# Performance work log

Hardware: AMD Instinct MI355X
Metric: run time of the kernel (lower is better)

The kernel has to match this reference:

```python
import jax, jax.numpy as jnp
import numpy as np
import math

ALPHA_MIN = math.exp(-1.0 / 5.0)   # ~0.8187
ALPHA_MAX = math.exp(-1.0 / 25.0)  # ~0.9608
THRESHOLD = 1.0


def setup_inputs() -> dict:
    key = jax.random.key(0)
    k1, k2, k3, k4, k5 = jax.random.split(key, 5)
    B, T, I, H = 32, 2048, 256, 512
    x = jax.random.normal(k1, (B, T, I), dtype=jnp.float32)
    # Linear weight, kaiming-ish scale
    W = jax.random.normal(k2, (H, I), dtype=jnp.float32) * (1.0 / np.sqrt(I))
    # alpha ~ U[exp(-1/5), exp(-1/25)] as in nn.init.uniform_
    alpha = ALPHA_MIN + jax.random.uniform(k3, (H,), dtype=jnp.float32) * (ALPHA_MAX - ALPHA_MIN)
    # initial membrane potential / spike state (torch.rand in _lif_cell)
    u0 = jax.random.uniform(k4, (B, H), dtype=jnp.float32)
    s0 = jax.random.uniform(k5, (B, H), dtype=jnp.float32)
    return {"x": x, "W": W, "alpha": alpha, "u0": u0, "s0": s0}


def reference(x, W, alpha, u0, s0):
    # clamp alpha to its admissible range (lif_feature has no 'NoClamp')
    alpha = jnp.clip(alpha, ALPHA_MIN, ALPHA_MAX)
    b = 1.0 - alpha  # lif_feature has no 'B'

    # feedforward projection: [B, T, H]
    Wx = jnp.einsum('bti,hi->bth', x, W)

    def step(carry, wx_t):
        ut, st = carry
        ut = alpha * (ut - st) + b * wx_t          # leaky integrate + soft reset
        st = (ut - THRESHOLD > 0).astype(ut.dtype)  # heaviside spike
        return (ut, st), st

    # scan over time: Wx -> [T, B, H]
    _, s = jax.lax.scan(step, (u0, s0), jnp.swapaxes(Wx, 0, 1))
    return jnp.swapaxes(s, 0, 1)  # [B, T, H]
```

## Files before the change

### kernel.cpp

```cpp
#include <hip/hip_runtime.h>
#include <hip/hip_bf16.h>

#define ALPHA_MIN 0.8187307530779818f
#define ALPHA_MAX 0.9607894391523232f

typedef _Float16 f16;
typedef _Float16 f16x8 __attribute__((ext_vector_type(8)));
typedef float f32x16 __attribute__((ext_vector_type(16)));

#define LDSTRIDE 40

__global__ __launch_bounds__(256, 2) void gemm_f16x3(
    const float* __restrict__ X,
    const float* __restrict__ W,
    float* __restrict__ C,
    int M, int N, int K)
{
    __shared__ f16 Ah[128 * LDSTRIDE];
    __shared__ f16 Al[128 * LDSTRIDE];
    __shared__ f16 Bh[128 * LDSTRIDE];
    __shared__ f16 Bl[128 * LDSTRIDE];

    const int tid = threadIdx.x;
    const int mt = blockIdx.x >> 2;
    const int nt = blockIdx.x & 3;
    const int m0 = mt * 128, n0 = nt * 128;

    const int lane = tid & 63;
    const int wv   = tid >> 6;
    const int wm   = wv & 1;
    const int wn   = wv >> 1;
    const int fm   = lane & 31;
    const int fq   = lane >> 5;

    const int srow = tid >> 2;
    const int sc8  = tid & 3;

    f32x16 accH[2][2], accL[2][2];
#pragma unroll
    for (int i = 0; i < 2; ++i)
#pragma unroll
        for (int j = 0; j < 2; ++j)
#pragma unroll
            for (int e = 0; e < 16; ++e) { accH[i][j][e] = 0.0f; accL[i][j][e] = 0.0f; }

    const int KT = K / 32;
    for (int kt = 0; kt < KT; ++kt) {
#pragma unroll
        for (int i = 0; i < 2; ++i) {
            const int row = srow + 64 * i;
            {
                const float* src = X + (size_t)(m0 + row) * K + kt * 32 + sc8 * 8;
                float4 v0 = *(const float4*)(src);
                float4 v1 = *(const float4*)(src + 4);
                float vin[8] = {v0.x, v0.y, v0.z, v0.w, v1.x, v1.y, v1.z, v1.w};
                f16x8 hv, lv;
#pragma unroll
                for (int j = 0; j < 8; ++j) {
                    f16 hj = (f16)vin[j];
                    hv[j] = hj;
                    lv[j] = (f16)((vin[j] - (float)hj) * 2048.0f);
                }
                *(f16x8*)&Ah[row * LDSTRIDE + sc8 * 8] = hv;
                *(f16x8*)&Al[row * LDSTRIDE + sc8 * 8] = lv;
            }
            {
                const float* src = W + (size_t)(n0 + row) * K + kt * 32 + sc8 * 8;
                float4 v0 = *(const float4*)(src);
                float4 v1 = *(const float4*)(src + 4);
                float vin[8] = {v0.x, v0.y, v0.z, v0.w, v1.x, v1.y, v1.z, v1.w};
                f16x8 hv, lv;
#pragma unroll
                for (int j = 0; j < 8; ++j) {
                    f16 hj = (f16)vin[j];
                    hv[j] = hj;
                    lv[j] = (f16)((vin[j] - (float)hj) * 2048.0f);
                }
                *(f16x8*)&Bh[row * LDSTRIDE + sc8 * 8] = hv;
                *(f16x8*)&Bl[row * LDSTRIDE + sc8 * 8] = lv;
            }
        }
        __syncthreads();

#pragma unroll
        for (int ks = 0; ks < 2; ++ks) {
            f16x8 af[2][2], bf[2][2];
#pragma unroll
            for (int mb = 0; mb < 2; ++mb) {
                const int ro = (wm * 64 + mb * 32 + fm) * LDSTRIDE + ks * 16 + fq * 8;
                af[mb][0] = *(const f16x8*)&Ah[ro];
                af[mb][1] = *(const f16x8*)&Al[ro];
            }
#pragma unroll
            for (int nb = 0; nb < 2; ++nb) {
                const int ro = (wn * 64 + nb * 32 + fm) * LDSTRIDE + ks * 16 + fq * 8;
                bf[nb][0] = *(const f16x8*)&Bh[ro];
                bf[nb][1] = *(const f16x8*)&Bl[ro];
            }
#pragma unroll
            for (int mb = 0; mb < 2; ++mb)
#pragma unroll
                for (int nb = 0; nb < 2; ++nb) {
                    accH[mb][nb] = __builtin_amdgcn_mfma_f32_32x32x16_f16(af[mb][0], bf[nb][0], accH[mb][nb], 0, 0, 0);
                    accL[mb][nb] = __builtin_amdgcn_mfma_f32_32x32x16_f16(af[mb][0], bf[nb][1], accL[mb][nb], 0, 0, 0);
                    accL[mb][nb] = __builtin_amdgcn_mfma_f32_32x32x16_f16(af[mb][1], bf[nb][0], accL[mb][nb], 0, 0, 0);
                }
        }
        __syncthreads();
    }

#pragma unroll
    for (int mb = 0; mb < 2; ++mb)
#pragma unroll
        for (int nb = 0; nb < 2; ++nb) {
            const int col   = n0 + wn * 64 + nb * 32 + fm;
            const int rbase = m0 + wm * 64 + mb * 32 + 4 * fq;
#pragma unroll
            for (int g = 0; g < 4; ++g)
#pragma unroll
                for (int r = 0; r < 4; ++r) {
                    const int row = rbase + 8 * g + r;
                    const float v = accH[mb][nb][4 * g + r]
                                  + accL[mb][nb][4 * g + r] * (1.0f / 2048.0f);
                    C[(size_t)row * N + col] = v;
                }
        }
}

#define SU 64

__global__ __launch_bounds__(64) void lif_scan(
    float* __restrict__ buf,
    const float* __restrict__ alpha,
    const float* __restrict__ u0,
    const float* __restrict__ s0,
    int T, int H)
{
    const int chain = blockIdx.x * 64 + threadIdx.x;
    const int h = chain % H;
    const int b = chain / H;

    float a = alpha[h];
    a = fminf(fmaxf(a, ALPHA_MIN), ALPHA_MAX);
    const float bb = 1.0f - a;

    float u = u0[chain];
    float s = s0[chain];

    float* base = buf + (size_t)b * T * H + h;

    float w0[SU], w1[SU];
#pragma unroll
    for (int j = 0; j < SU; ++j) w0[j] = base[(size_t)j * H];

    const int NC = T / SU;
    for (int c = 0; c < NC; c += 2) {
#pragma unroll
        for (int j = 0; j < SU; ++j) w1[j] = base[(size_t)((c + 1) * SU + j) * H];
#pragma unroll
        for (int j = 0; j < SU; ++j) {
            const float d = u - s;
            u = fmaf(a, d, bb * w0[j]);
            s = (u > 1.0f) ? 1.0f : 0.0f;
            base[(size_t)(c * SU + j) * H] = s;
        }
        if (c + 2 < NC) {
#pragma unroll
            for (int j = 0; j < SU; ++j) w0[j] = base[(size_t)((c + 2) * SU + j) * H];
        }
#pragma unroll
        for (int j = 0; j < SU; ++j) {
            const float d = u - s;
            u = fmaf(a, d, bb * w1[j]);
            s = (u > 1.0f) ? 1.0f : 0.0f;
            base[(size_t)((c + 1) * SU + j) * H] = s;
        }
    }
}

extern "C" void kernel_launch(void* const* d_in, const int* in_sizes, int n_in,
                              void* d_out, int out_size, void* d_ws, size_t ws_size,
                              hipStream_t stream) {
    const float* x     = (const float*)d_in[0];
    const float* W     = (const float*)d_in[1];
    const float* alpha = (const float*)d_in[2];
    const float* u0    = (const float*)d_in[3];
    const float* s0    = (const float*)d_in[4];
    float* out = (float*)d_out;

    const int H = in_sizes[2];
    const int I = in_sizes[1] / H;
    const int B = in_sizes[3] / H;
    const int T = in_sizes[0] / (B * I);
    const int M = B * T;

    const int grid = (M / 128) * (H / 128);
    gemm_f16x3<<<grid, 256, 0, stream>>>(x, W, out, M, H, I);

    lif_scan<<<(B * H) / 64, 64, 0, stream>>>(out, alpha, u0, s0, T, H);
}
```

Baseline: 302.9 us.

## Pre-split inputs into fp16 hi/lo buffers before GEMM, scan out-of-place

```diff
diff --git a/kernel.cpp b/kernel.cpp
--- a/kernel.cpp
+++ b/kernel.cpp
@@ -8,13 +8,32 @@
 typedef _Float16 f16x8 __attribute__((ext_vector_type(8)));
 typedef float f32x16 __attribute__((ext_vector_type(16)));
 
+__global__ __launch_bounds__(256) void convert_split(
+    const float* __restrict__ src,
+    f16* __restrict__ hi, f16* __restrict__ lo, int n8)
+{
+    const int i = blockIdx.x * 256 + threadIdx.x;
+    if (i >= n8) return;
+    const float4 v0 = ((const float4*)src)[2 * i];
+    const float4 v1 = ((const float4*)src)[2 * i + 1];
+    const float v[8] = {v0.x, v0.y, v0.z, v0.w, v1.x, v1.y, v1.z, v1.w};
+    f16x8 h, l;
+#pragma unroll
+    for (int j = 0; j < 8; ++j) {
+        const f16 hj = (f16)v[j];
+        h[j] = hj;
+        l[j] = (f16)((v[j] - (float)hj) * 2048.0f);
+    }
+    ((f16x8*)hi)[i] = h;
+    ((f16x8*)lo)[i] = l;
+}
+
 #define LDSTRIDE 40
 
-__global__ __launch_bounds__(256, 2) void gemm_f16x3(
-    const float* __restrict__ X,
-    const float* __restrict__ W,
-    float* __restrict__ C,
-    int M, int N, int K)
+__global__ __launch_bounds__(256, 2) void gemm_f16pre(
+    const f16* __restrict__ Xh, const f16* __restrict__ Xl,
+    const f16* __restrict__ Wh, const f16* __restrict__ Wl,
+    float* __restrict__ C, int M, int N, int K)
 {
     __shared__ f16 Ah[128 * LDSTRIDE];
     __shared__ f16 Al[128 * LDSTRIDE];
@@ -49,36 +68,13 @@
 #pragma unroll
         for (int i = 0; i < 2; ++i) {
             const int row = srow + 64 * i;
-            {
-                const float* src = X + (size_t)(m0 + row) * K + kt * 32 + sc8 * 8;
-                float4 v0 = *(const float4*)(src);
-                float4 v1 = *(const float4*)(src + 4);
-                float vin[8] = {v0.x, v0.y, v0.z, v0.w, v1.x, v1.y, v1.z, v1.w};
-                f16x8 hv, lv;
-#pragma unroll
-                for (int j = 0; j < 8; ++j) {
-                    f16 hj = (f16)vin[j];
-                    hv[j] = hj;
-                    lv[j] = (f16)((vin[j] - (float)hj) * 2048.0f);
-                }
-                *(f16x8*)&Ah[row * LDSTRIDE + sc8 * 8] = hv;
-                *(f16x8*)&Al[row * LDSTRIDE + sc8 * 8] = lv;
-            }
-            {
-                const float* src = W + (size_t)(n0 + row) * K + kt * 32 + sc8 * 8;
-                float4 v0 = *(const float4*)(src);
-                float4 v1 = *(const float4*)(src + 4);
-                float vin[8] = {v0.x, v0.y, v0.z, v0.w, v1.x, v1.y, v1.z, v1.w};
-                f16x8 hv, lv;
-#pragma unroll
-                for (int j = 0; j < 8; ++j) {
-                    f16 hj = (f16)vin[j];
-                    hv[j] = hj;
-                    lv[j] = (f16)((vin[j] - (float)hj) * 2048.0f);
-                }
-                *(f16x8*)&Bh[row * LDSTRIDE + sc8 * 8] = hv;
-                *(f16x8*)&Bl[row * LDSTRIDE + sc8 * 8] = lv;
-            }
+            const size_t gx = (size_t)(m0 + row) * K + kt * 32 + sc8 * 8;
+            const size_t gw = (size_t)(n0 + row) * K + kt * 32 + sc8 * 8;
+            const int lo_ = row * LDSTRIDE + sc8 * 8;
+            *(f16x8*)&Ah[lo_] = *(const f16x8*)&Xh[gx];
+            *(f16x8*)&Al[lo_] = *(const f16x8*)&Xl[gx];
+            *(f16x8*)&Bh[lo_] = *(const f16x8*)&Wh[gw];
+            *(f16x8*)&Bl[lo_] = *(const f16x8*)&Wl[gw];
         }
         __syncthreads();
 
@@ -120,17 +116,17 @@
 #pragma unroll
                 for (int r = 0; r < 4; ++r) {
                     const int row = rbase + 8 * g + r;
-                    const float v = accH[mb][nb][4 * g + r]
-                                  + accL[mb][nb][4 * g + r] * (1.0f / 2048.0f);
-                    C[(size_t)row * N + col] = v;
-                }
-        }
-}
-
-#define SU 64
-
-__global__ __launch_bounds__(64) void lif_scan(
-    float* __restrict__ buf,
+                    C[(size_t)row * N + col] = accH[mb][nb][4 * g + r]
+                                             + accL[mb][nb][4 * g + r] * (1.0f / 2048.0f);
+                }
+        }
+}
+
+#define SU 32
+
+__global__ __launch_bounds__(64) void lif_scan2(
+    const float* __restrict__ wx,
+    float* __restrict__ out,
     const float* __restrict__ alpha,
     const float* __restrict__ u0,
     const float* __restrict__ s0,
@@ -147,33 +143,159 @@
     float u = u0[chain];
     float s = s0[chain];
 
-    float* base = buf + (size_t)b * T * H + h;
+    const float* src = wx + (size_t)b * T * H + h;
+    float* dst = out + (size_t)b * T * H + h;
 
     float w0[SU], w1[SU];
 #pragma unroll
-    for (int j = 0; j < SU; ++j) w0[j] = base[(size_t)j * H];
+    for (int j = 0; j < SU; ++j) w0[j] = src[(size_t)j * H];
 
     const int NC = T / SU;
     for (int c = 0; c < NC; c += 2) {
 #pragma unroll
-        for (int j = 0; j < SU; ++j) w1[j] = base[(size_t)((c + 1) * SU + j) * H];
+        for (int j = 0; j < SU; ++j) w1[j] = src[(size_t)((c + 1) * SU + j) * H];
 #pragma unroll
         for (int j = 0; j < SU; ++j) {
-            const float d = u - s;
-            u = fmaf(a, d, bb * w0[j]);
+            u = fmaf(a, u - s, bb * w0[j]);
             s = (u > 1.0f) ? 1.0f : 0.0f;
-            base[(size_t)(c * SU + j) * H] = s;
+            dst[(size_t)(c * SU + j) * H] = s;
         }
         if (c + 2 < NC) {
 #pragma unroll
-            for (int j = 0; j < SU; ++j) w0[j] = base[(size_t)((c + 2) * SU + j) * H];
+            for (int j = 0; j < SU; ++j) w0[j] = src[(size_t)((c + 2) * SU + j) * H];
         }
 #pragma unroll
         for (int j = 0; j < SU; ++j) {
-            const float d = u - s;
-            u = fmaf(a, d, bb * w1[j]);
+            u = fmaf(a, u - s, bb * w1[j]);
             s = (u > 1.0f) ? 1.0f : 0.0f;
-            base[(size_t)((c + 1) * SU + j) * H] = s;
+            dst[(size_t)((c + 1) * SU + j) * H] = s;
+        }
+    }
+}
+
+__global__ __launch_bounds__(256, 2) void gemm_f16x3(
+    const float* __restrict__ X, const float* __restrict__ W,
+    float* __restrict__ C, int M, int N, int K)
+{
+    __shared__ f16 Ah[128 * LDSTRIDE];
+    __shared__ f16 Al[128 * LDSTRIDE];
+    __shared__ f16 Bh[128 * LDSTRIDE];
+    __shared__ f16 Bl[128 * LDSTRIDE];
+
+    const int tid = threadIdx.x;
+    const int mt = blockIdx.x >> 2;
+    const int nt = blockIdx.x & 3;
+    const int m0 = mt * 128, n0 = nt * 128;
+    const int lane = tid & 63;
+    const int wv = tid >> 6, wm = wv & 1, wn = wv >> 1;
+    const int fm = lane & 31, fq = lane >> 5;
+    const int srow = tid >> 2, sc8 = tid & 3;
+
+    f32x16 accH[2][2], accL[2][2];
+#pragma unroll
+    for (int i = 0; i < 2; ++i)
+#pragma unroll
+        for (int j = 0; j < 2; ++j)
+#pragma unroll
+            for (int e = 0; e < 16; ++e) { accH[i][j][e] = 0.0f; accL[i][j][e] = 0.0f; }
+
+    const int KT = K / 32;
+    for (int kt = 0; kt < KT; ++kt) {
+#pragma unroll
+        for (int i = 0; i < 2; ++i) {
+            const int row = srow + 64 * i;
+            {
+                const float* srcp = X + (size_t)(m0 + row) * K + kt * 32 + sc8 * 8;
+                float4 v0 = *(const float4*)(srcp);
+                float4 v1 = *(const float4*)(srcp + 4);
+                float vin[8] = {v0.x, v0.y, v0.z, v0.w, v1.x, v1.y, v1.z, v1.w};
+                f16x8 hv, lv;
+#pragma unroll
+                for (int j = 0; j < 8; ++j) {
+                    f16 hj = (f16)vin[j];
+                    hv[j] = hj; lv[j] = (f16)((vin[j] - (float)hj) * 2048.0f);
+                }
+                *(f16x8*)&Ah[row * LDSTRIDE + sc8 * 8] = hv;
+                *(f16x8*)&Al[row * LDSTRIDE + sc8 * 8] = lv;
+            }
+            {
+                const float* srcp = W + (size_t)(n0 + row) * K + kt * 32 + sc8 * 8;
+                float4 v0 = *(const float4*)(srcp);
+                float4 v1 = *(const float4*)(srcp + 4);
+                float vin[8] = {v0.x, v0.y, v0.z, v0.w, v1.x, v1.y, v1.z, v1.w};
+                f16x8 hv, lv;
+#pragma unroll
+                for (int j = 0; j < 8; ++j) {
+                    f16 hj = (f16)vin[j];
+                    hv[j] = hj; lv[j] = (f16)((vin[j] - (float)hj) * 2048.0f);
+                }
+                *(f16x8*)&Bh[row * LDSTRIDE + sc8 * 8] = hv;
+                *(f16x8*)&Bl[row * LDSTRIDE + sc8 * 8] = lv;
+            }
+        }
+        __syncthreads();
+#pragma unroll
+        for (int ks = 0; ks < 2; ++ks) {
+            f16x8 af[2][2], bf[2][2];
+#pragma unroll
+            for (int mb = 0; mb < 2; ++mb) {
+                const int ro = (wm * 64 + mb * 32 + fm) * LDSTRIDE + ks * 16 + fq * 8;
+                af[mb][0] = *(const f16x8*)&Ah[ro];
+                af[mb][1] = *(const f16x8*)&Al[ro];
+            }
+#pragma unroll
+            for (int nb = 0; nb < 2; ++nb) {
+                const int ro = (wn * 64 + nb * 32 + fm) * LDSTRIDE + ks * 16 + fq * 8;
+                bf[nb][0] = *(const f16x8*)&Bh[ro];
+                bf[nb][1] = *(const f16x8*)&Bl[ro];
+            }
+#pragma unroll
+            for (int mb = 0; mb < 2; ++mb)
+#pragma unroll
+                for (int nb = 0; nb < 2; ++nb) {
+                    accH[mb][nb] = __builtin_amdgcn_mfma_f32_32x32x16_f16(af[mb][0], bf[nb][0], accH[mb][nb], 0, 0, 0);
+                    accL[mb][nb] = __builtin_amdgcn_mfma_f32_32x32x16_f16(af[mb][0], bf[nb][1], accL[mb][nb], 0, 0, 0);
+                    accL[mb][nb] = __builtin_amdgcn_mfma_f32_32x32x16_f16(af[mb][1], bf[nb][0], accL[mb][nb], 0, 0, 0);
+                }
+        }
+        __syncthreads();
+    }
+#pragma unroll
+    for (int mb = 0; mb < 2; ++mb)
+#pragma unroll
+        for (int nb = 0; nb < 2; ++nb) {
+            const int col   = n0 + wn * 64 + nb * 32 + fm;
+            const int rbase = m0 + wm * 64 + mb * 32 + 4 * fq;
+#pragma unroll
+            for (int g = 0; g < 4; ++g)
+#pragma unroll
+                for (int r = 0; r < 4; ++r)
+                    C[(size_t)(rbase + 8 * g + r) * N + col] =
+                        accH[mb][nb][4 * g + r] + accL[mb][nb][4 * g + r] * (1.0f / 2048.0f);
+        }
+}
+
+__global__ __launch_bounds__(64) void lif_scan_inplace(
+    float* __restrict__ buf, const float* __restrict__ alpha,
+    const float* __restrict__ u0, const float* __restrict__ s0, int T, int H)
+{
+    const int chain = blockIdx.x * 64 + threadIdx.x;
+    const int h = chain % H;
+    const int b = chain / H;
+    float a = alpha[h];
+    a = fminf(fmaxf(a, ALPHA_MIN), ALPHA_MAX);
+    const float bb = 1.0f - a;
+    float u = u0[chain], s = s0[chain];
+    float* base = buf + (size_t)b * T * H + h;
+    for (int t0 = 0; t0 < T; t0 += SU) {
+        float w[SU];
+#pragma unroll
+        for (int j = 0; j < SU; ++j) w[j] = base[(size_t)(t0 + j) * H];
+#pragma unroll
+        for (int j = 0; j < SU; ++j) {
+            u = fmaf(a, u - s, bb * w[j]);
+            s = (u > 1.0f) ? 1.0f : 0.0f;
+            base[(size_t)(t0 + j) * H] = s;
         }
     }
 }
@@ -194,8 +316,29 @@
     const int T = in_sizes[0] / (B * I);
     const int M = B * T;
 
-    const int grid = (M / 128) * (H / 128);
-    gemm_f16x3<<<grid, 256, 0, stream>>>(x, W, out, M, H, I);
-
-    lif_scan<<<(B * H) / 64, 64, 0, stream>>>(out, alpha, u0, s0, T, H);
-}
+    const size_t szX16 = (size_t)M * I * sizeof(f16);
+    const size_t szW16 = (size_t)H * I * sizeof(f16);
+    const size_t szWx  = (size_t)M * H * sizeof(float);
+    const size_t need  = szWx + 2 * szX16 + 2 * szW16;
+
+    if (ws_size >= need) {
+        char* p = (char*)d_ws;
+        float* Wx = (float*)p;               p += szWx;
+        f16* Xh = (f16*)p;                   p += szX16;
+        f16* Xl = (f16*)p;                   p += szX16;
+        f16* Wh = (f16*)p;                   p += szW16;
+        f16* Wl = (f16*)p;
+
+        const int n8x = M * I / 8;
+        const int n8w = H * I / 8;
+        convert_split<<<(n8x + 255) / 256, 256, 0, stream>>>(x, Xh, Xl, n8x);
+        convert_split<<<(n8w + 255) / 256, 256, 0, stream>>>(W, Wh, Wl, n8w);
+
+        gemm_f16pre<<<(M / 128) * (H / 128), 256, 0, stream>>>(Xh, Xl, Wh, Wl, Wx, M, H, I);
+
+        lif_scan2<<<(B * H) / 64, 64, 0, stream>>>(Wx, out, alpha, u0, s0, T, H);
+    } else {
+        gemm_f16x3<<<(M / 128) * (H / 128), 256, 0, stream>>>(x, W, out, M, H, I);
+        lif_scan_inplace<<<(B * H) / 64, 64, 0, stream>>>(out, alpha, u0, s0, T, H);
+    }
+}
```

Result: slower. 319.1 us (+5.4%).

## Double-buffer GEMM LDS tiles and write scan output to separate buffer

Applied to the files above, without the earlier changes.

```diff
diff --git a/kernel.cpp b/kernel.cpp
--- a/kernel.cpp
+++ b/kernel.cpp
@@ -10,16 +10,16 @@
 
 #define LDSTRIDE 40
 
-__global__ __launch_bounds__(256, 2) void gemm_f16x3(
+__global__ __launch_bounds__(256, 2) void gemm_fused(
     const float* __restrict__ X,
     const float* __restrict__ W,
     float* __restrict__ C,
     int M, int N, int K)
 {
-    __shared__ f16 Ah[128 * LDSTRIDE];
-    __shared__ f16 Al[128 * LDSTRIDE];
-    __shared__ f16 Bh[128 * LDSTRIDE];
-    __shared__ f16 Bl[128 * LDSTRIDE];
+    __shared__ f16 Ah[2][128 * LDSTRIDE];
+    __shared__ f16 Al[2][128 * LDSTRIDE];
+    __shared__ f16 Bh[2][128 * LDSTRIDE];
+    __shared__ f16 Bl[2][128 * LDSTRIDE];
 
     const int tid = threadIdx.x;
     const int mt = blockIdx.x >> 2;
@@ -36,6 +36,11 @@
     const int srow = tid >> 2;
     const int sc8  = tid & 3;
 
+    const float* px0 = X + (size_t)(m0 + srow)      * K + sc8 * 8;
+    const float* px1 = X + (size_t)(m0 + srow + 64) * K + sc8 * 8;
+    const float* pw0 = W + (size_t)(n0 + srow)      * K + sc8 * 8;
+    const float* pw1 = W + (size_t)(n0 + srow + 64) * K + sc8 * 8;
+
     f32x16 accH[2][2], accL[2][2];
 #pragma unroll
     for (int i = 0; i < 2; ++i)
@@ -44,43 +49,51 @@
 #pragma unroll
             for (int e = 0; e < 16; ++e) { accH[i][j][e] = 0.0f; accL[i][j][e] = 0.0f; }
 
+    float4 t[2][4];
+
+    auto issue_loads = [&](int kt) {
+        const int o = kt * 32;
+        t[0][0] = *(const float4*)(px0 + o);
+        t[0][1] = *(const float4*)(px0 + o + 4);
+        t[0][2] = *(const float4*)(pw0 + o);
+        t[0][3] = *(const float4*)(pw0 + o + 4);
+        t[1][0] = *(const float4*)(px1 + o);
+        t[1][1] = *(const float4*)(px1 + o + 4);
+        t[1][2] = *(const float4*)(pw1 + o);
+        t[1][3] = *(const float4*)(pw1 + o + 4);
+    };
+
+    auto write_lds = [&](int buf) {
+#pragma unroll
+        for (int i = 0; i < 2; ++i) {
+            const int off = (srow + 64 * i) * LDSTRIDE + sc8 * 8;
+            const float vx[8] = {t[i][0].x, t[i][0].y, t[i][0].z, t[i][0].w,
+                                 t[i][1].x, t[i][1].y, t[i][1].z, t[i][1].w};
+            const float vw[8] = {t[i][2].x, t[i][2].y, t[i][2].z, t[i][2].w,
+                                 t[i][3].x, t[i][3].y, t[i][3].z, t[i][3].w};
+            f16x8 xh, xl, wh, wl;
+#pragma unroll
+            for (int j = 0; j < 8; ++j) {
+                const f16 hx = (f16)vx[j];
+                xh[j] = hx; xl[j] = (f16)((vx[j] - (float)hx) * 2048.0f);
+                const f16 hw = (f16)vw[j];
+                wh[j] = hw; wl[j] = (f16)((vw[j] - (float)hw) * 2048.0f);
+            }
+            *(f16x8*)&Ah[buf][off] = xh;
+            *(f16x8*)&Al[buf][off] = xl;
+            *(f16x8*)&Bh[buf][off] = wh;
+            *(f16x8*)&Bl[buf][off] = wl;
+        }
+    };
+
     const int KT = K / 32;
+    issue_loads(0);
+    write_lds(0);
+    __syncthreads();
+
     for (int kt = 0; kt < KT; ++kt) {
-#pragma unroll
-        for (int i = 0; i < 2; ++i) {
-            const int row = srow + 64 * i;
-            {
-                const float* src = X + (size_t)(m0 + row) * K + kt * 32 + sc8 * 8;
-                float4 v0 = *(const float4*)(src);
-                float4 v1 = *(const float4*)(src + 4);
-                float vin[8] = {v0.x, v0.y, v0.z, v0.w, v1.x, v1.y, v1.z, v1.w};
-                f16x8 hv, lv;
-#pragma unroll
-                for (int j = 0; j < 8; ++j) {
-                    f16 hj = (f16)vin[j];
-                    hv[j] = hj;
-                    lv[j] = (f16)((vin[j] - (float)hj) * 2048.0f);
-                }
-                *(f16x8*)&Ah[row * LDSTRIDE + sc8 * 8] = hv;
-                *(f16x8*)&Al[row * LDSTRIDE + sc8 * 8] = lv;
-            }
-            {
-                const float* src = W + (size_t)(n0 + row) * K + kt * 32 + sc8 * 8;
-                float4 v0 = *(const float4*)(src);
-                float4 v1 = *(const float4*)(src + 4);
-                float vin[8] = {v0.x, v0.y, v0.z, v0.w, v1.x, v1.y, v1.z, v1.w};
-                f16x8 hv, lv;
-#pragma unroll
-                for (int j = 0; j < 8; ++j) {
-                    f16 hj = (f16)vin[j];
-                    hv[j] = hj;
-                    lv[j] = (f16)((vin[j] - (float)hj) * 2048.0f);
-                }
-                *(f16x8*)&Bh[row * LDSTRIDE + sc8 * 8] = hv;
-                *(f16x8*)&Bl[row * LDSTRIDE + sc8 * 8] = lv;
-            }
-        }
-        __syncthreads();
+        const int cur = kt & 1;
+        if (kt + 1 < KT) issue_loads(kt + 1);
 
 #pragma unroll
         for (int ks = 0; ks < 2; ++ks) {
@@ -88,14 +101,14 @@
 #pragma unroll
             for (int mb = 0; mb < 2; ++mb) {
                 const int ro = (wm * 64 + mb * 32 + fm) * LDSTRIDE + ks * 16 + fq * 8;
-                af[mb][0] = *(const f16x8*)&Ah[ro];
-                af[mb][1] = *(const f16x8*)&Al[ro];
+                af[mb][0] = *(const f16x8*)&Ah[cur][ro];
+                af[mb][1] = *(const f16x8*)&Al[cur][ro];
             }
 #pragma unroll
             for (int nb = 0; nb < 2; ++nb) {
                 const int ro = (wn * 64 + nb * 32 + fm) * LDSTRIDE + ks * 16 + fq * 8;
-                bf[nb][0] = *(const f16x8*)&Bh[ro];
-                bf[nb][1] = *(const f16x8*)&Bl[ro];
+                bf[nb][0] = *(const f16x8*)&Bh[cur][ro];
+                bf[nb][1] = *(const f16x8*)&Bl[cur][ro];
             }
 #pragma unroll
             for (int mb = 0; mb < 2; ++mb)
@@ -106,6 +119,8 @@
                     accL[mb][nb] = __builtin_amdgcn_mfma_f32_32x32x16_f16(af[mb][1], bf[nb][0], accL[mb][nb], 0, 0, 0);
                 }
         }
+
+        if (kt + 1 < KT) write_lds(cur ^ 1);
         __syncthreads();
     }
 
@@ -120,17 +135,17 @@
 #pragma unroll
                 for (int r = 0; r < 4; ++r) {
                     const int row = rbase + 8 * g + r;
-                    const float v = accH[mb][nb][4 * g + r]
-                                  + accL[mb][nb][4 * g + r] * (1.0f / 2048.0f);
-                    C[(size_t)row * N + col] = v;
+                    C[(size_t)row * N + col] = accH[mb][nb][4 * g + r]
+                                             + accL[mb][nb][4 * g + r] * (1.0f / 2048.0f);
                 }
         }
 }
 
 #define SU 64
 
-__global__ __launch_bounds__(64) void lif_scan(
-    float* __restrict__ buf,
+__global__ __launch_bounds__(64) void lif_scan2(
+    const float* __restrict__ wx,
+    float* __restrict__ out,
     const float* __restrict__ alpha,
     const float* __restrict__ u0,
     const float* __restrict__ s0,
@@ -147,33 +162,57 @@
     float u = u0[chain];
     float s = s0[chain];
 
-    float* base = buf + (size_t)b * T * H + h;
+    const float* src = wx + (size_t)b * T * H + h;
+    float* dst = out + (size_t)b * T * H + h;
 
     float w0[SU], w1[SU];
 #pragma unroll
-    for (int j = 0; j < SU; ++j) w0[j] = base[(size_t)j * H];
+    for (int j = 0; j < SU; ++j) w0[j] = src[(size_t)j * H];
 
     const int NC = T / SU;
     for (int c = 0; c < NC; c += 2) {
 #pragma unroll
-        for (int j = 0; j < SU; ++j) w1[j] = base[(size_t)((c + 1) * SU + j) * H];
+        for (int j = 0; j < SU; ++j) w1[j] = src[(size_t)((c + 1) * SU + j) * H];
 #pragma unroll
         for (int j = 0; j < SU; ++j) {
-            const float d = u - s;
-            u = fmaf(a, d, bb * w0[j]);
+            u = fmaf(a, u - s, bb * w0[j]);
             s = (u > 1.0f) ? 1.0f : 0.0f;
-            base[(size_t)(c * SU + j) * H] = s;
+            __builtin_nontemporal_store(s, &dst[(size_t)(c * SU + j) * H]);
         }
         if (c + 2 < NC) {
 #pragma unroll
-            for (int j = 0; j < SU; ++j) w0[j] = base[(size_t)((c + 2) * SU + j) * H];
+            for (int j = 0; j < SU; ++j) w0[j] = src[(size_t)((c + 2) * SU + j) * H];
         }
 #pragma unroll
         for (int j = 0; j < SU; ++j) {
-            const float d = u - s;
-            u = fmaf(a, d, bb * w1[j]);
+            u = fmaf(a, u - s, bb * w1[j]);
             s = (u > 1.0f) ? 1.0f : 0.0f;
-            base[(size_t)((c + 1) * SU + j) * H] = s;
+            __builtin_nontemporal_store(s, &dst[(size_t)((c + 1) * SU + j) * H]);
+        }
+    }
+}
+
+__global__ __launch_bounds__(64) void lif_scan_inplace(
+    float* __restrict__ buf, const float* __restrict__ alpha,
+    const float* __restrict__ u0, const float* __restrict__ s0, int T, int H)
+{
+    const int chain = blockIdx.x * 64 + threadIdx.x;
+    const int h = chain % H;
+    const int b = chain / H;
+    float a = alpha[h];
+    a = fminf(fmaxf(a, ALPHA_MIN), ALPHA_MAX);
+    const float bb = 1.0f - a;
+    float u = u0[chain], s = s0[chain];
+    float* base = buf + (size_t)b * T * H + h;
+    for (int t0 = 0; t0 < T; t0 += 32) {
+        float w[32];
+#pragma unroll
+        for (int j = 0; j < 32; ++j) w[j] = base[(size_t)(t0 + j) * H];
+#pragma unroll
+        for (int j = 0; j < 32; ++j) {
+            u = fmaf(a, u - s, bb * w[j]);
+            s = (u > 1.0f) ? 1.0f : 0.0f;
+            base[(size_t)(t0 + j) * H] = s;
         }
     }
 }
@@ -194,8 +233,14 @@
     const int T = in_sizes[0] / (B * I);
     const int M = B * T;
 
-    const int grid = (M / 128) * (H / 128);
-    gemm_f16x3<<<grid, 256, 0, stream>>>(x, W, out, M, H, I);
-
-    lif_scan<<<(B * H) / 64, 64, 0, stream>>>(out, alpha, u0, s0, T, H);
-}
+    const size_t szWx = (size_t)M * H * sizeof(float);
+
+    if (ws_size >= szWx) {
+        float* Wx = (float*)d_ws;
+        gemm_fused<<<(M / 128) * (H / 128), 256, 0, stream>>>(x, W, Wx, M, H, I);
+        lif_scan2<<<(B * H) / 64, 64, 0, stream>>>(Wx, out, alpha, u0, s0, T, H);
+    } else {
+        gemm_fused<<<(M / 128) * (H / 128), 256, 0, stream>>>(x, W, out, M, H, I);
+        lif_scan_inplace<<<(B * H) / 64, 64, 0, stream>>>(out, alpha, u0, s0, T, H);
+    }
+}
```

Measured after the change: 302.3 us. No clear change (-0.2%).
